# Kernel optimization log

Hardware: AMD Instinct MI355X
Metric: run time of the kernel (lower is better)

## Reference

```python
import jax, jax.numpy as jnp
import numpy as np

P, N, A = 8, 160, 32            # poses, blocks per pose, atoms per block (tile size)
BT = 24                         # number of block types
MAX_DON, MAX_ACC = 4, 8         # max donor-H / acceptor slots per block tile
ND, NAT = 16, 16                # donor / acceptor chemical types
NPAIR = ND * NAT                # donor-type x acceptor-type pair table size
NPOLY = 11                      # degree-10 polynomial: 11 coefficients
MIN_SEP = 4                     # minimum bond separation for an hbond


def setup_inputs() -> dict:
    key = jax.random.key(0)
    ks = jax.random.split(key, 12)
    coords = jax.random.normal(ks[0], (P, N * A, 3), jnp.float32) * 10.0
    # dispatch every ordered block pair in every pose: (pose, block1, block2)
    pp, bb1, bb2 = jnp.meshgrid(jnp.arange(P), jnp.arange(N), jnp.arange(N), indexing="ij")
    block_pair_dispatch_indices = jnp.stack(
        [pp.ravel(), bb1.ravel(), bb2.ravel()], axis=-1
    ).astype(jnp.int32)
    pose_stack_block_coord_offset = jnp.tile(
        (jnp.arange(N, dtype=jnp.int32) * A)[None, :], (P, 1)
    )
    pose_stack_block_type = jax.random.randint(ks[1], (P, N), 0, BT, jnp.int32)
    pose_stack_min_bond_separation = jax.random.randint(ks[2], (P, N, N), 0, 6, jnp.int32)
    bt_tile_n_donH = jax.random.randint(ks[3], (BT,), 0, MAX_DON + 1, jnp.int32)
    bt_tile_n_acc = jax.random.randint(ks[4], (BT,), 0, MAX_ACC + 1, jnp.int32)
    bt_tile_donH_inds = jax.random.randint(ks[5], (BT, MAX_DON), 0, A, jnp.int32)
    bt_tile_acc_inds = jax.random.randint(ks[6], (BT, MAX_ACC), 0, A, jnp.int32)
    bt_tile_donor_type = jax.random.randint(ks[7], (BT, MAX_DON), 0, ND, jnp.int32)
    bt_tile_acceptor_type = jax.random.randint(ks[8], (BT, MAX_ACC), 0, NAT, jnp.int32)
    bt_tile_acceptor_hybridization = jax.random.randint(ks[9], (BT, MAX_ACC), 0, 3, jnp.int32)
    pair_params = jax.random.uniform(ks[10], (NPAIR, 3), jnp.float32, 0.5, 1.5)
    pair_polynomials = jax.random.normal(ks[11], (NPAIR, NPOLY), jnp.float32) * 0.01
    # [max_AH_distance, min_energy_clamp, unused, unused]
    global_params = jnp.array([6.0, -2.0, 0.0, 1.0], jnp.float32)
    return dict(
        coords=coords,
        block_pair_dispatch_indices=block_pair_dispatch_indices,
        pose_stack_block_coord_offset=pose_stack_block_coord_offset,
        pose_stack_block_type=pose_stack_block_type,
        pose_stack_min_bond_separation=pose_stack_min_bond_separation,
        bt_tile_n_donH=bt_tile_n_donH,
        bt_tile_n_acc=bt_tile_n_acc,
        bt_tile_donH_inds=bt_tile_donH_inds,
        bt_tile_acc_inds=bt_tile_acc_inds,
        bt_tile_donor_type=bt_tile_donor_type,
        bt_tile_acceptor_type=bt_tile_acceptor_type,
        bt_tile_acceptor_hybridization=bt_tile_acceptor_hybridization,
        pair_params=pair_params,
        pair_polynomials=pair_polynomials,
        global_params=global_params,
    )


def reference(coords, block_pair_dispatch_indices, pose_stack_block_coord_offset,
              pose_stack_block_type, pose_stack_min_bond_separation,
              bt_tile_n_donH, bt_tile_n_acc, bt_tile_donH_inds, bt_tile_acc_inds,
              bt_tile_donor_type, bt_tile_acceptor_type,
              bt_tile_acceptor_hybridization, pair_params, pair_polynomials,
              global_params):
    p = block_pair_dispatch_indices[:, 0]   # [K]
    b1 = block_pair_dispatch_indices[:, 1]
    b2 = block_pair_dispatch_indices[:, 2]
    bt1 = pose_stack_block_type[p, b1]      # [K] block type of donor block
    bt2 = pose_stack_block_type[p, b2]      # [K] block type of acceptor block
    off1 = pose_stack_block_coord_offset[p, b1]
    off2 = pose_stack_block_coord_offset[p, b2]

    don_atoms = bt_tile_donH_inds[bt1]      # [K, MD] donor-H atom slots
    acc_atoms = bt_tile_acc_inds[bt2]       # [K, MA] acceptor atom slots
    H = coords[p[:, None], off1[:, None] + don_atoms]   # [K, MD, 3]
    Ac = coords[p[:, None], off2[:, None] + acc_atoms]  # [K, MA, 3]

    # AH distances for every donor-H x acceptor candidate in the pair
    diff = H[:, :, None, :] - Ac[:, None, :, :]          # [K, MD, MA, 3]
    d = jnp.sqrt(jnp.sum(diff * diff, axis=-1) + 1e-12)  # [K, MD, MA]

    # pair-type index into the donor_type x acceptor_type tables
    pt = bt_tile_donor_type[bt1][:, :, None] * NAT + bt_tile_acceptor_type[bt2][:, None, :]

    # Horner evaluation of the degree-10 AH-distance polynomial; gather one
    # coefficient column per step to avoid a [K, MD, MA, 11] intermediate.
    e = pair_polynomials[pt, 0]
    for c in range(1, NPOLY):
        e = e * d + pair_polynomials[pt, c]

    # hybridization-dependent weight (sp2 / sp3 / ring)
    hyb = jnp.broadcast_to(bt_tile_acceptor_hybridization[bt2][:, None, :], pt.shape)
    w = pair_params[pt, hyb]                              # [K, MD, MA]

    # validity: slot within donor/acceptor counts, distinct blocks,
    # sufficient bond separation, within distance cutoff
    don_valid = jnp.arange(MAX_DON)[None, :] < bt_tile_n_donH[bt1][:, None]
    acc_valid = jnp.arange(MAX_ACC)[None, :] < bt_tile_n_acc[bt2][:, None]
    pair_ok = (b1 != b2) & (pose_stack_min_bond_separation[p, b1, b2] >= MIN_SEP)
    valid = (don_valid[:, :, None] & acc_valid[:, None, :]
             & pair_ok[:, None, None] & (d < global_params[0]))

    e = jnp.maximum(jnp.minimum(e, 0.0), global_params[1])  # clamp to [min_E, 0]
    energy = jnp.where(valid, w * e, 0.0)                    # [K, MD, MA]

    # scatter-accumulate per-pair energies into per-pose totals
    pose_energies = jax.ops.segment_sum(
        jnp.sum(energy, axis=(1, 2)), p, num_segments=P)     # [P]
    return pose_energies
```

## Files before the change

kernel.cpp:

```cpp
#include <hip/hip_runtime.h>

#define NP 8
#define NB 160
#define NA 32
#define NATYPE 16
#define NPOLY 11
#define MIN_SEP 4
#define DVALID (1 << 16)

__global__ __launch_bounds__(256) void hbond_main(
    const float* __restrict__ coords,
    const int*   __restrict__ coord_off,
    const int*   __restrict__ block_type,
    const int*   __restrict__ min_sep,
    const int*   __restrict__ n_donH,
    const int*   __restrict__ n_acc,
    const int*   __restrict__ donH_inds,
    const int*   __restrict__ acc_inds,
    const int*   __restrict__ donor_type,
    const int*   __restrict__ acceptor_type,
    const int*   __restrict__ acceptor_hyb,
    const float* __restrict__ pair_params,
    const float* __restrict__ pair_poly,
    const float* __restrict__ gp,
    float*       __restrict__ partials)
{
    const int t  = threadIdx.x;
    const int p  = blockIdx.x / NB;
    const int b1 = blockIdx.x - p * NB;

    __shared__ int4  b2info[NB];
    __shared__ int   b2list[NB];
    __shared__ int   wc[4];
    __shared__ float wsum[4];

    const float cut  = gp[0];
    const float emin = gp[1];

    bool ok = false;
    if (t < NB) {
        const int bt2  = block_type[p * NB + t];
        const int off2 = coord_off[p * NB + t];
        const int na   = n_acc[bt2];
        ok = (t != b1) && (min_sep[(p * NB + b1) * NB + t] >= MIN_SEP);
        b2info[t] = make_int4(bt2, off2, na, 0);
    }

    const int bt1  = block_type[p * NB + b1];
    const int off1 = coord_off[p * NB + b1];
    const int nd   = n_donH[bt1];
    float4 dv[4];
    #pragma unroll
    for (int dn = 0; dn < 4; ++dn) {
        const int hatom = donH_inds[bt1 * 4 + dn];
        const int dbase = donor_type[bt1 * 4 + dn] * NATYPE;
        const float* Hc = coords + (size_t)(p * (NB * NA) + off1 + hatom) * 3;
        dv[dn] = make_float4(Hc[0], Hc[1], Hc[2],
                             __int_as_float((dbase & 0xff) | ((dn < nd) ? DVALID : 0)));
    }

    const unsigned long long m = __ballot(ok);
    const int wv = t >> 6, ln = t & 63;
    if (ln == 0) wc[wv] = __popcll(m);
    __syncthreads();

    int pre = 0, cnt = 0;
    #pragma unroll
    for (int w = 0; w < 4; ++w) {
        cnt += wc[w];
        if (w < wv) pre += wc[w];
    }
    if (ok) b2list[pre + __popcll(m & ((1ull << ln) - 1ull))] = t;
    __syncthreads();

    float energy = 0.0f;
    const int cnt8 = cnt * 8;
    for (int i = t; i < cnt8; i += 256) {
        const int b2 = b2list[i >> 3];
        const int a  = i & 7;
        const int4 info = b2info[b2];

        float hd0 = 0, hd1 = 0, hd2 = 0, hd3 = 0;
        int   hp0 = 0, hp1 = 0, hp2 = 0, hp3 = 0;
        int   nh = 0, hyb = 0;

        if (a < info.z) {
            const int ai    = acc_inds[info.x * 8 + a];
            const int atype = acceptor_type[info.x * 8 + a];
            hyb             = acceptor_hyb[info.x * 8 + a];
            const float* Ac = coords + (size_t)(p * (NB * NA) + info.y + ai) * 3;
            const float ax = Ac[0], ay = Ac[1], az = Ac[2];

            #pragma unroll
            for (int dn = 0; dn < 4; ++dn) {
                const int dbits = __float_as_int(dv[dn].w);
                if (!(dbits & DVALID)) continue;
                const float dx = dv[dn].x - ax;
                const float dy = dv[dn].y - ay;
                const float dz = dv[dn].z - az;
                const float dd = sqrtf(dx * dx + dy * dy + dz * dz + 1e-12f);
                if (dd < cut) {
                    const int pp = (dbits & 0xff) + atype;
                    hd3 = (nh == 3) ? dd : hd3;  hp3 = (nh == 3) ? pp : hp3;
                    hd2 = (nh == 2) ? dd : hd2;  hp2 = (nh == 2) ? pp : hp2;
                    hd1 = (nh == 1) ? dd : hd1;  hp1 = (nh == 1) ? pp : hp1;
                    hd0 = (nh == 0) ? dd : hd0;  hp0 = (nh == 0) ? pp : hp0;
                    ++nh;
                }
            }
        }

        #pragma unroll
        for (int h = 0; h < 4; ++h) {
            if (!__any(h < nh)) break;
            if (h < nh) {
                const float dd = (h == 0) ? hd0 : (h == 1) ? hd1 : (h == 2) ? hd2 : hd3;
                const int   pp = (h == 0) ? hp0 : (h == 1) ? hp1 : (h == 2) ? hp2 : hp3;
                const float* c = pair_poly + pp * NPOLY;
                float ev = c[0];
                #pragma unroll
                for (int k = 1; k < NPOLY; ++k) ev = ev * dd + c[k];
                const float w = pair_params[pp * 3 + hyb];
                ev = fmaxf(fminf(ev, 0.0f), emin);
                energy += w * ev;
            }
        }
    }

    #pragma unroll
    for (int off = 32; off >= 1; off >>= 1)
        energy += __shfl_down(energy, off, 64);
    if (ln == 0) wsum[wv] = energy;
    __syncthreads();
    if (t == 0) partials[blockIdx.x] = wsum[0] + wsum[1] + wsum[2] + wsum[3];
}

__global__ __launch_bounds__(256) void hbond_reduce(
    const float* __restrict__ partials, float* __restrict__ out)
{
    const int wv = threadIdx.x >> 6, ln = threadIdx.x & 63;
    #pragma unroll
    for (int q = 0; q < 2; ++q) {
        const int pose = wv * 2 + q;
        const float* base = partials + pose * NB;
        float v = base[ln] + base[64 + ln] + ((ln < 32) ? base[128 + ln] : 0.0f);
        #pragma unroll
        for (int off = 32; off >= 1; off >>= 1)
            v += __shfl_down(v, off, 64);
        if (ln == 0) out[pose] = v;
    }
}

extern "C" void kernel_launch(void* const* d_in, const int* in_sizes, int n_in,
                              void* d_out, int out_size, void* d_ws, size_t ws_size,
                              hipStream_t stream) {
    const float* coords        = (const float*)d_in[0];
    const int*   coord_off     = (const int*)  d_in[2];
    const int*   block_type    = (const int*)  d_in[3];
    const int*   min_sep       = (const int*)  d_in[4];
    const int*   n_donH        = (const int*)  d_in[5];
    const int*   n_acc         = (const int*)  d_in[6];
    const int*   donH_inds     = (const int*)  d_in[7];
    const int*   acc_inds      = (const int*)  d_in[8];
    const int*   donor_type    = (const int*)  d_in[9];
    const int*   acceptor_type = (const int*)  d_in[10];
    const int*   acceptor_hyb  = (const int*)  d_in[11];
    const float* pair_params   = (const float*)d_in[12];
    const float* pair_poly     = (const float*)d_in[13];
    const float* gp            = (const float*)d_in[14];
    float*       partials      = (float*)d_ws;
    float*       out           = (float*)d_out;

    hbond_main<<<NP * NB, 256, 0, stream>>>(
        coords, coord_off, block_type, min_sep,
        n_donH, n_acc, donH_inds, acc_inds,
        donor_type, acceptor_type, acceptor_hyb,
        pair_params, pair_poly, gp, partials);

    hbond_reduce<<<1, 256, 0, stream>>>(partials, out);
}
```

Baseline: 12.19 us.

## Fuse per-pose reduction into main kernel via tagged-slot spin-wait in block 0

Drops the separate reduce kernel launch. Each workgroup now writes its partial sum to a 64-bit workspace slot tagged with a magic word. Workgroup 0 polls all slots until every tag appears, sums per pose, writes the output and clears the slots for the next call. This removes the second launch and its inter-kernel gap. In exchange, workgroup 0 busy-waits on a CU and relies on all other workgroups being scheduled while it spins; it also assumes the workspace does not already hold the magic tag from stale data.

```diff
diff --git a/kernel.cpp b/kernel.cpp
--- a/kernel.cpp
+++ b/kernel.cpp
@@ -7,8 +7,10 @@
 #define NPOLY 11
 #define MIN_SEP 4
 #define DVALID (1 << 16)
-
-__global__ __launch_bounds__(256) void hbond_main(
+#define NWG (NP * NB)
+#define MAGICU 0x48424F4Eu
+
+__global__ __launch_bounds__(256) void hbond_kernel(
     const float* __restrict__ coords,
     const int*   __restrict__ coord_off,
     const int*   __restrict__ block_type,
@@ -23,7 +25,8 @@
     const float* __restrict__ pair_params,
     const float* __restrict__ pair_poly,
     const float* __restrict__ gp,
-    float*       __restrict__ partials)
+    unsigned long long* __restrict__ slots,
+    float*       __restrict__ out)
 {
     const int t  = threadIdx.x;
     const int p  = blockIdx.x / NB;
@@ -132,22 +135,42 @@
         energy += __shfl_down(energy, off, 64);
     if (ln == 0) wsum[wv] = energy;
     __syncthreads();
-    if (t == 0) partials[blockIdx.x] = wsum[0] + wsum[1] + wsum[2] + wsum[3];
-}
-
-__global__ __launch_bounds__(256) void hbond_reduce(
-    const float* __restrict__ partials, float* __restrict__ out)
-{
-    const int wv = threadIdx.x >> 6, ln = threadIdx.x & 63;
-    #pragma unroll
-    for (int q = 0; q < 2; ++q) {
-        const int pose = wv * 2 + q;
-        const float* base = partials + pose * NB;
-        float v = base[ln] + base[64 + ln] + ((ln < 32) ? base[128 + ln] : 0.0f);
+    if (t == 0) {
+        const float s = wsum[0] + wsum[1] + wsum[2] + wsum[3];
+        const unsigned long long v =
+            ((unsigned long long)MAGICU << 32) |
+            (unsigned long long)(unsigned int)__float_as_int(s);
+        __hip_atomic_store(&slots[blockIdx.x], v,
+                           __ATOMIC_RELAXED, __HIP_MEMORY_SCOPE_AGENT);
+    }
+
+    if (blockIdx.x == 0) {
         #pragma unroll
-        for (int off = 32; off >= 1; off >>= 1)
-            v += __shfl_down(v, off, 64);
-        if (ln == 0) out[pose] = v;
+        for (int q = 0; q < 2; ++q) {
+            const int pose = wv * 2 + q;
+            unsigned long long* base = slots + pose * NB;
+            float acc = 0.0f;
+            #pragma unroll
+            for (int r = 0; r < 3; ++r) {
+                const int idx = r * 64 + ln;
+                if (idx < NB) {
+                    unsigned long long v;
+                    for (;;) {
+                        v = __hip_atomic_load(&base[idx], __ATOMIC_RELAXED,
+                                              __HIP_MEMORY_SCOPE_AGENT);
+                        if ((unsigned int)(v >> 32) == MAGICU) break;
+                        __builtin_amdgcn_s_sleep(1);
+                    }
+                    acc += __int_as_float((int)(unsigned int)(v & 0xffffffffull));
+                    __hip_atomic_store(&base[idx], 0ull,
+                                       __ATOMIC_RELAXED, __HIP_MEMORY_SCOPE_AGENT);
+                }
+            }
+            #pragma unroll
+            for (int off = 32; off >= 1; off >>= 1)
+                acc += __shfl_down(acc, off, 64);
+            if (ln == 0) out[pose] = acc;
+        }
     }
 }
 
@@ -168,14 +191,12 @@
     const float* pair_params   = (const float*)d_in[12];
     const float* pair_poly     = (const float*)d_in[13];
     const float* gp            = (const float*)d_in[14];
-    float*       partials      = (float*)d_ws;
+    unsigned long long* slots  = (unsigned long long*)d_ws;
     float*       out           = (float*)d_out;
 
-    hbond_main<<<NP * NB, 256, 0, stream>>>(
+    hbond_kernel<<<NWG, 256, 0, stream>>>(
         coords, coord_off, block_type, min_sep,
         n_donH, n_acc, donH_inds, acc_inds,
         donor_type, acceptor_type, acceptor_hyb,
-        pair_params, pair_poly, gp, partials);
-
-    hbond_reduce<<<1, 256, 0, stream>>>(partials, out);
+        pair_params, pair_poly, gp, slots, out);
 }
```

Result: slower. 12.96 us (+6.3%).

## Process two donor blocks per workgroup and write per-wave partials

Applied to the files above, without the earlier changes.

Each workgroup now handles two consecutive donor blocks (b1) rather than one, so the grid shrinks from 1280 to 640 workgroups. The shared b2 block info setup is loaded once and reused for both donor blocks, and each has its own compacted acceptor list processed in sequence. The final block-level reduction through shared memory and its barrier is removed: each wave writes its own partial, and the reduce kernel sums 320 values per pose. The aim is to amortise per-workgroup setup and launch overhead, at the cost of fewer workgroups to spread across CUs and a serial two-segment loop per workgroup.

```diff
diff --git a/kernel.cpp b/kernel.cpp
--- a/kernel.cpp
+++ b/kernel.cpp
@@ -7,6 +7,9 @@
 #define NPOLY 11
 #define MIN_SEP 4
 #define DVALID (1 << 16)
+#define NBT 2
+#define NWG_PER_POSE (NB / NBT)
+#define NWG (NP * NWG_PER_POSE)
 
 __global__ __launch_bounds__(256) void hbond_main(
     const float* __restrict__ coords,
@@ -25,114 +28,128 @@
     const float* __restrict__ gp,
     float*       __restrict__ partials)
 {
-    const int t  = threadIdx.x;
-    const int p  = blockIdx.x / NB;
-    const int b1 = blockIdx.x - p * NB;
-
-    __shared__ int4  b2info[NB];
-    __shared__ int   b2list[NB];
-    __shared__ int   wc[4];
-    __shared__ float wsum[4];
+    const int t   = threadIdx.x;
+    const int p   = blockIdx.x / NWG_PER_POSE;
+    const int pr  = blockIdx.x - p * NWG_PER_POSE;
+    const int b1a = pr * NBT, b1b = b1a + 1;
+
+    __shared__ int4 b2info[NB];
+    __shared__ int  b2listA[NB];
+    __shared__ int  b2listB[NB];
+    __shared__ int  wcA[4], wcB[4];
 
     const float cut  = gp[0];
     const float emin = gp[1];
 
-    bool ok = false;
+    bool okA = false, okB = false;
     if (t < NB) {
         const int bt2  = block_type[p * NB + t];
         const int off2 = coord_off[p * NB + t];
         const int na   = n_acc[bt2];
-        ok = (t != b1) && (min_sep[(p * NB + b1) * NB + t] >= MIN_SEP);
+        okA = (t != b1a) && (min_sep[(p * NB + b1a) * NB + t] >= MIN_SEP);
+        okB = (t != b1b) && (min_sep[(p * NB + b1b) * NB + t] >= MIN_SEP);
         b2info[t] = make_int4(bt2, off2, na, 0);
     }
 
-    const int bt1  = block_type[p * NB + b1];
-    const int off1 = coord_off[p * NB + b1];
-    const int nd   = n_donH[bt1];
-    float4 dv[4];
-    #pragma unroll
-    for (int dn = 0; dn < 4; ++dn) {
-        const int hatom = donH_inds[bt1 * 4 + dn];
-        const int dbase = donor_type[bt1 * 4 + dn] * NATYPE;
-        const float* Hc = coords + (size_t)(p * (NB * NA) + off1 + hatom) * 3;
-        dv[dn] = make_float4(Hc[0], Hc[1], Hc[2],
-                             __int_as_float((dbase & 0xff) | ((dn < nd) ? DVALID : 0)));
-    }
-
-    const unsigned long long m = __ballot(ok);
+    float4 dA[4], dB[4];
+    {
+        const int bt1a = block_type[p * NB + b1a], bt1b = block_type[p * NB + b1b];
+        const int off1a = coord_off[p * NB + b1a], off1b = coord_off[p * NB + b1b];
+        const int nda = n_donH[bt1a], ndb = n_donH[bt1b];
+        #pragma unroll
+        for (int dn = 0; dn < 4; ++dn) {
+            const float* Ha = coords + (size_t)(p * (NB * NA) + off1a + donH_inds[bt1a * 4 + dn]) * 3;
+            const float* Hb = coords + (size_t)(p * (NB * NA) + off1b + donH_inds[bt1b * 4 + dn]) * 3;
+            dA[dn] = make_float4(Ha[0], Ha[1], Ha[2],
+                __int_as_float(((donor_type[bt1a * 4 + dn] * NATYPE) & 0xff) | ((dn < nda) ? DVALID : 0)));
+            dB[dn] = make_float4(Hb[0], Hb[1], Hb[2],
+                __int_as_float(((donor_type[bt1b * 4 + dn] * NATYPE) & 0xff) | ((dn < ndb) ? DVALID : 0)));
+        }
+    }
+
+    const unsigned long long mA = __ballot(okA);
+    const unsigned long long mB = __ballot(okB);
     const int wv = t >> 6, ln = t & 63;
-    if (ln == 0) wc[wv] = __popcll(m);
+    if (ln == 0) { wcA[wv] = __popcll(mA); wcB[wv] = __popcll(mB); }
     __syncthreads();
 
-    int pre = 0, cnt = 0;
+    int preA = 0, preB = 0, cntA = 0, cntB = 0;
     #pragma unroll
     for (int w = 0; w < 4; ++w) {
-        cnt += wc[w];
-        if (w < wv) pre += wc[w];
-    }
-    if (ok) b2list[pre + __popcll(m & ((1ull << ln) - 1ull))] = t;
+        cntA += wcA[w]; cntB += wcB[w];
+        if (w < wv) { preA += wcA[w]; preB += wcB[w]; }
+    }
+    {
+        const unsigned long long below = (1ull << ln) - 1ull;
+        if (okA) b2listA[preA + __popcll(mA & below)] = t;
+        if (okB) b2listB[preB + __popcll(mB & below)] = t;
+    }
     __syncthreads();
 
     float energy = 0.0f;
-    const int cnt8 = cnt * 8;
-    for (int i = t; i < cnt8; i += 256) {
-        const int b2 = b2list[i >> 3];
-        const int a  = i & 7;
-        const int4 info = b2info[b2];
-
-        float hd0 = 0, hd1 = 0, hd2 = 0, hd3 = 0;
-        int   hp0 = 0, hp1 = 0, hp2 = 0, hp3 = 0;
-        int   nh = 0, hyb = 0;
-
-        if (a < info.z) {
-            const int ai    = acc_inds[info.x * 8 + a];
-            const int atype = acceptor_type[info.x * 8 + a];
-            hyb             = acceptor_hyb[info.x * 8 + a];
-            const float* Ac = coords + (size_t)(p * (NB * NA) + info.y + ai) * 3;
-            const float ax = Ac[0], ay = Ac[1], az = Ac[2];
+    #pragma unroll 1
+    for (int seg = 0; seg < 2; ++seg) {
+        const int cnt8 = (seg ? cntB : cntA) * 8;
+        const int* __restrict__ list = seg ? b2listB : b2listA;
+        const float4* dv = seg ? dB : dA;
+
+        for (int i = t; i < cnt8; i += 256) {
+            const int b2 = list[i >> 3];
+            const int a  = i & 7;
+            const int4 info = b2info[b2];
+
+            float hd0 = 0, hd1 = 0, hd2 = 0, hd3 = 0;
+            int   hp0 = 0, hp1 = 0, hp2 = 0, hp3 = 0;
+            int   nh = 0, hyb = 0;
+
+            if (a < info.z) {
+                const int ai    = acc_inds[info.x * 8 + a];
+                const int atype = acceptor_type[info.x * 8 + a];
+                hyb             = acceptor_hyb[info.x * 8 + a];
+                const float* Ac = coords + (size_t)(p * (NB * NA) + info.y + ai) * 3;
+                const float ax = Ac[0], ay = Ac[1], az = Ac[2];
+
+                #pragma unroll
+                for (int dn = 0; dn < 4; ++dn) {
+                    const int dbits = __float_as_int(dv[dn].w);
+                    if (!(dbits & DVALID)) continue;
+                    const float dx = dv[dn].x - ax;
+                    const float dy = dv[dn].y - ay;
+                    const float dz = dv[dn].z - az;
+                    const float dd = sqrtf(dx * dx + dy * dy + dz * dz + 1e-12f);
+                    if (dd < cut) {
+                        const int pp = (dbits & 0xff) + atype;
+                        hd3 = (nh == 3) ? dd : hd3;  hp3 = (nh == 3) ? pp : hp3;
+                        hd2 = (nh == 2) ? dd : hd2;  hp2 = (nh == 2) ? pp : hp2;
+                        hd1 = (nh == 1) ? dd : hd1;  hp1 = (nh == 1) ? pp : hp1;
+                        hd0 = (nh == 0) ? dd : hd0;  hp0 = (nh == 0) ? pp : hp0;
+                        ++nh;
+                    }
+                }
+            }
 
             #pragma unroll
-            for (int dn = 0; dn < 4; ++dn) {
-                const int dbits = __float_as_int(dv[dn].w);
-                if (!(dbits & DVALID)) continue;
-                const float dx = dv[dn].x - ax;
-                const float dy = dv[dn].y - ay;
-                const float dz = dv[dn].z - az;
-                const float dd = sqrtf(dx * dx + dy * dy + dz * dz + 1e-12f);
-                if (dd < cut) {
-                    const int pp = (dbits & 0xff) + atype;
-                    hd3 = (nh == 3) ? dd : hd3;  hp3 = (nh == 3) ? pp : hp3;
-                    hd2 = (nh == 2) ? dd : hd2;  hp2 = (nh == 2) ? pp : hp2;
-                    hd1 = (nh == 1) ? dd : hd1;  hp1 = (nh == 1) ? pp : hp1;
-                    hd0 = (nh == 0) ? dd : hd0;  hp0 = (nh == 0) ? pp : hp0;
-                    ++nh;
+            for (int h = 0; h < 4; ++h) {
+                if (!__any(h < nh)) break;
+                if (h < nh) {
+                    const float dd = (h == 0) ? hd0 : (h == 1) ? hd1 : (h == 2) ? hd2 : hd3;
+                    const int   pp = (h == 0) ? hp0 : (h == 1) ? hp1 : (h == 2) ? hp2 : hp3;
+                    const float* c = pair_poly + pp * NPOLY;
+                    float ev = c[0];
+                    #pragma unroll
+                    for (int kk = 1; kk < NPOLY; ++kk) ev = ev * dd + c[kk];
+                    const float w = pair_params[pp * 3 + hyb];
+                    ev = fmaxf(fminf(ev, 0.0f), emin);
+                    energy += w * ev;
                 }
             }
         }
-
-        #pragma unroll
-        for (int h = 0; h < 4; ++h) {
-            if (!__any(h < nh)) break;
-            if (h < nh) {
-                const float dd = (h == 0) ? hd0 : (h == 1) ? hd1 : (h == 2) ? hd2 : hd3;
-                const int   pp = (h == 0) ? hp0 : (h == 1) ? hp1 : (h == 2) ? hp2 : hp3;
-                const float* c = pair_poly + pp * NPOLY;
-                float ev = c[0];
-                #pragma unroll
-                for (int k = 1; k < NPOLY; ++k) ev = ev * dd + c[k];
-                const float w = pair_params[pp * 3 + hyb];
-                ev = fmaxf(fminf(ev, 0.0f), emin);
-                energy += w * ev;
-            }
-        }
     }
 
     #pragma unroll
     for (int off = 32; off >= 1; off >>= 1)
         energy += __shfl_down(energy, off, 64);
-    if (ln == 0) wsum[wv] = energy;
-    __syncthreads();
-    if (t == 0) partials[blockIdx.x] = wsum[0] + wsum[1] + wsum[2] + wsum[3];
+    if (ln == 0) partials[blockIdx.x * 4 + wv] = energy;
 }
 
 __global__ __launch_bounds__(256) void hbond_reduce(
@@ -142,8 +159,10 @@
     #pragma unroll
     for (int q = 0; q < 2; ++q) {
         const int pose = wv * 2 + q;
-        const float* base = partials + pose * NB;
-        float v = base[ln] + base[64 + ln] + ((ln < 32) ? base[128 + ln] : 0.0f);
+        const float* base = partials + pose * NWG_PER_POSE * 4;
+        float v = 0.0f;
+        #pragma unroll
+        for (int r = 0; r < 5; ++r) v += base[r * 64 + ln];
         #pragma unroll
         for (int off = 32; off >= 1; off >>= 1)
             v += __shfl_down(v, off, 64);
@@ -171,7 +190,7 @@
     float*       partials      = (float*)d_ws;
     float*       out           = (float*)d_out;
 
-    hbond_main<<<NP * NB, 256, 0, stream>>>(
+    hbond_main<<<NWG, 256, 0, stream>>>(
         coords, coord_off, block_type, min_sep,
         n_donH, n_acc, donH_inds, acc_inds,
         donor_type, acceptor_type, acceptor_hyb,
```

Result: slower. 14.55 us (+19.3%).
